# Kernel tuning notes

Measured on AMD Instinct MI355X. Metric: run time of the kernel, lower is better.

Reference implementation:

```python
import jax, jax.numpy as jnp
import numpy as np

BOHR = 1.8897261258369282  # Angstrom -> Bohr, as in SKparam
CUTOFF = 6.0
LATTICE = np.diag([5.0, 5.0, 5.0]).astype(np.float32)
N_ATOMS, N_SPECIES, N_POLY, N_KPT = 512, 4, 12, 32


def _compute_shifts():
    # Exact replica of DFTB.compute_shift in numpy.
    inv = np.linalg.inv(LATTICE)
    n_rep = np.ceil(np.linalg.norm(inv, axis=0) * CUTOFF).astype(int)
    grid = np.stack(np.meshgrid(*[np.arange(-n, n + 1) for n in n_rep], indexing='ij'), -1).reshape(-1, 3)
    a = np.where(grid > 0, grid - 1, grid)
    shrunk = np.where(a < 0, grid + 1, a)              # shrink each component toward 0 by 1
    sh2 = shrunk.astype(np.float32) @ LATTICE           # lattice.T @ r == r @ lattice
    keep = np.linalg.norm(sh2, axis=1) < CUTOFF
    return (grid[keep].astype(np.float32) @ LATTICE)    # [S,3], S=81 for this lattice/cutoff


def setup_inputs() -> dict:
    key = jax.random.key(0)
    k1, k2, k3, k4, k5 = jax.random.split(key, 5)
    positions = jax.random.uniform(k1, (N_ATOMS, 3), dtype=jnp.float32) * 5.0
    species = jax.random.randint(k2, (N_ATOMS,), 0, N_SPECIES)
    kpoints = jax.random.uniform(k3, (N_KPT, 3), dtype=jnp.float32)
    # decaying per-degree scale keeps polyval bounded at x = cutoff*BOHR ~ 11.3
    scale = (1.0 / 12.0) ** jnp.arange(N_POLY, dtype=jnp.float32)
    param_matrix = jax.random.normal(k4, (N_SPECIES, N_SPECIES, N_POLY), dtype=jnp.float32) * scale
    onsite = jax.random.normal(k5, (N_SPECIES,), dtype=jnp.float32)
    shifts = jnp.asarray(_compute_shifts())
    return {"positions": positions, "species": species, "kpoints": kpoints,
            "param_matrix": param_matrix, "onsite": onsite, "shifts": shifts}


def reference(positions, species, kpoints, param_matrix, onsite, shifts):
    # pairwise distance vectors under periodic shifts: [N,N,S,3]
    dvec = positions[None, :, None, :] + shifts[None, None, :, :] - positions[:, :, None][:, None].reshape(-1, 1, 1, 3)
    dvec = positions[None, :, None, :] + shifts[None, None, :, :] - positions[:, None, None, :]
    dr2 = jnp.sum(dvec * dvec, axis=-1)                       # [N,N,S]
    dr = jnp.sqrt(jnp.where(dr2 > 0.0, dr2, 1.0))
    dr = jnp.where(dr2 > 0.0, dr, 0.0)
    x = dr * BOHR
    # species-pair gather of Vsss polynomial coefficients: [N,N,P]
    coeffs = param_matrix[species[:, None], species[None, :]]
    # Horner eval (torch polyval: p[0] is the constant term after fliplr)
    y = jnp.zeros_like(x)
    for k in range(N_POLY - 1, -1, -1):
        y = y * x + coeffs[:, :, k][:, :, None]
    # calc_tb_params mask: zero for onsite (dr<=0.1) and beyond cutoff
    V = jnp.where((dr > 0.1) & (dr <= CUTOFF), y, 0.0)        # [N,N,S]
    # Bloch phases per k-point and shift (calc_phase_matrix, vectorized)
    inv_lat = jnp.asarray(np.linalg.inv(LATTICE))
    kc = kpoints @ inv_lat.T                                   # [K,3]
    ang = (2.0 * np.pi) * (kc @ shifts.T)                      # [K,S]
    Hr = jnp.einsum('ijs,ks->kij', V, jnp.cos(ang))            # [K,N,N]
    Hi = jnp.einsum('ijs,ks->kij', V, jnp.sin(ang))
    Hr = Hr + jnp.diag(onsite[species])[None]                  # onsite diagonal
    return jnp.stack([Hr, Hi])                                 # [2,K,N,N] real view of complex H
```

## Files before the change

kernel.cpp:

```cpp
#include <hip/hip_runtime.h>

#define NATOMS 512
#define N2 (NATOMS*NATOMS)
#define NKPT 32
#define NPOLY 12
#define NSP 4
#define NSMAX 96
#define TJ 256
#define NTHREADS 256
#define SG_STR 260

typedef __attribute__((ext_vector_type(8))) short bf16x8;
typedef __attribute__((ext_vector_type(4))) float f32x4;

static __device__ __forceinline__ unsigned f2bf2(float lo, float hi) {
    union { float f; unsigned u; } a, b; a.f = lo; b.f = hi;
    unsigned ra = a.u + 0x7FFFu + ((a.u >> 16) & 1u);
    unsigned rb = b.u + 0x7FFFu + ((b.u >> 16) & 1u);
    return (ra >> 16) | (rb & 0xFFFF0000u);
}

__global__ void phase_tab(const float* __restrict__ kpoints,
                          const float* __restrict__ shifts,
                          unsigned* __restrict__ Ttg, int ns)
{
    int idx = blockIdx.x * 256 + threadIdx.x;
    if (idx >= 64 * 48) return;
    int row = idx / 48, s2 = idx - row * 48;
    int k = row & 31;
    float kcx = kpoints[k*3]   * 0.2f;
    float kcy = kpoints[k*3+1] * 0.2f;
    float kcz = kpoints[k*3+2] * 0.2f;
    float val[2] = {0.f, 0.f};
    #pragma unroll
    for (int h = 0; h < 2; ++h) {
        int s = 2*s2 + h;
        if (s < ns) {
            float d = (kcx*shifts[s*3] + kcy*shifts[s*3+1]) + kcz*shifts[s*3+2];
            float sn, cs;
            sincosf(6.283185307179586f * d, &sn, &cs);
            val[h] = (row >= 32) ? sn : cs;
        }
    }
    Ttg[idx] = f2bf2(val[0], val[1]);
}

__global__ __launch_bounds__(NTHREADS, 4)
void dftb4(const float* __restrict__ positions,
           const int* __restrict__ species,
           const float* __restrict__ param,
           const float* __restrict__ onsite,
           const float* __restrict__ shifts,
           const unsigned short* __restrict__ Ttg,
           float* __restrict__ out, int ns)
{
    __shared__ float Sg[16][SG_STR];
    __shared__ float4 sh4p[NSMAX + NSMAX/8];
    __shared__ float cpar4[NPOLY*NSP];
    __shared__ float4 pjs[TJ];
    __shared__ int sjs[TJ];

    const int tid = threadIdx.x;
    const int bi = blockIdx.x >> 1;
    const int jt = blockIdx.x & 1;
    if (ns > NSMAX) ns = NSMAX;

    const int si = species[bi];

    {
        int j = jt*TJ + tid;
        pjs[tid] = make_float4(positions[j*3], positions[j*3+1], positions[j*3+2], 0.f);
        sjs[tid] = species[j];
    }
    if (tid < NPOLY*NSP) {
        int q = tid >> 2, sj = tid & 3;
        cpar4[tid] = param[(si*NSP + sj)*NPOLY + q];
    }
    for (int s = tid; s < NSMAX; s += NTHREADS) {
        float4 v = (s < ns)
            ? make_float4(shifts[s*3], shifts[s*3+1], shifts[s*3+2], 0.f)
            : make_float4(1e9f, 1e9f, 1e9f, 0.f);
        sh4p[s + (s >> 3)] = v;
    }
    __syncthreads();

    const int lane = tid & 63, w = tid >> 6;
    const int r16 = lane & 15, g = lane >> 4;

    const float pix = positions[bi*3], piy = positions[bi*3+1], piz = positions[bi*3+2];
    const float ons = onsite[si];

    bf16x8 A[4][3];
    #pragma unroll
    for (int mf = 0; mf < 4; ++mf) {
        const int jl = w*64 + mf*16 + r16;
        const float4 pj = pjs[jl];
        const int sj = sjs[jl];
        float c[NPOLY];
        #pragma unroll
        for (int q = 0; q < NPOLY; ++q) c[q] = cpar4[q*4 + sj];

        #pragma unroll
        for (int kf = 0; kf < 3; ++kf) {
            unsigned pk[4];
            #pragma unroll
            for (int e2 = 0; e2 < 4; ++e2) {
                float v[2];
                #pragma unroll
                for (int h = 0; h < 2; ++h) {
                    const int s = kf*32 + g*8 + e2*2 + h;
                    float4 sh = sh4p[s + (s >> 3)];
                    float dx = (pj.x + sh.x) - pix;
                    float dy = (pj.y + sh.y) - piy;
                    float dz = (pj.z + sh.z) - piz;
                    float dr2 = (__fmul_rn(dx,dx) + __fmul_rn(dy,dy)) + __fmul_rn(dz,dz);
                    float v_ = 0.f;
                    if (dr2 <= 36.001f) {
                        float dr = sqrtf(dr2);
                        if (dr > 0.1f && dr <= 6.0f) {
                            float x = dr * 1.8897261258369282f;
                            float y = c[NPOLY-1];
                            #pragma unroll
                            for (int q = NPOLY-2; q >= 0; --q) y = fmaf(y, x, c[q]);
                            v_ = y;
                        }
                    }
                    v[h] = v_;
                }
                pk[e2] = f2bf2(v[0], v[1]);
            }
            union { unsigned u[4]; bf16x8 v; } au;
            au.u[0] = pk[0]; au.u[1] = pk[1]; au.u[2] = pk[2]; au.u[3] = pk[3];
            A[mf][kf] = au.v;
        }
    }

    const size_t obase = (size_t)bi*NATOMS + (size_t)jt*TJ;
    #pragma unroll
    for (int nf = 0; nf < 4; ++nf) {
        const unsigned short* tb = Ttg + (size_t)(nf*16 + r16)*NSMAX + g*8;
        bf16x8 B0 = *(const bf16x8*)(tb);
        bf16x8 B1 = *(const bf16x8*)(tb + 32);
        bf16x8 B2 = *(const bf16x8*)(tb + 64);

        f32x4 acc[4];
        #pragma unroll
        for (int mf = 0; mf < 4; ++mf) {
            acc[mf] = (f32x4){0.f, 0.f, 0.f, 0.f};
            acc[mf] = __builtin_amdgcn_mfma_f32_16x16x32_bf16(A[mf][0], B0, acc[mf], 0, 0, 0);
            acc[mf] = __builtin_amdgcn_mfma_f32_16x16x32_bf16(A[mf][1], B1, acc[mf], 0, 0, 0);
            acc[mf] = __builtin_amdgcn_mfma_f32_16x16x32_bf16(A[mf][2], B2, acc[mf], 0, 0, 0);
        }

        __syncthreads();
        #pragma unroll
        for (int mf = 0; mf < 4; ++mf)
            *(float4*)&Sg[r16][w*64 + mf*16 + g*4] = *(float4*)&acc[mf];
        __syncthreads();

        #pragma unroll
        for (int q = 0; q < 4; ++q) {
            const int p = w*4 + q;
            const int kcol = nf*16 + p;
            float4 v = *(float4*)&Sg[p][lane*4];
            if (kcol < 32) {
                int d = bi - (int)(jt*TJ + lane*4);
                if (d >= 0 && d < 4) ((float*)&v)[d] += ons;
            }
            *(float4*)(out + (size_t)kcol*N2 + obase + lane*4) = v;
        }
    }
}

extern "C" void kernel_launch(void* const* d_in, const int* in_sizes, int n_in,
                              void* d_out, int out_size, void* d_ws, size_t ws_size,
                              hipStream_t stream) {
    const float* positions = (const float*)d_in[0];
    const int*   species   = (const int*)d_in[1];
    const float* kpoints   = (const float*)d_in[2];
    const float* param     = (const float*)d_in[3];
    const float* onsite    = (const float*)d_in[4];
    const float* shifts    = (const float*)d_in[5];
    int ns = in_sizes[5] / 3;
    float* out = (float*)d_out;
    unsigned* Ttg = (unsigned*)d_ws;

    phase_tab<<<dim3(12), 256, 0, stream>>>(kpoints, shifts, Ttg, ns);
    dim3 grid(NATOMS * (NATOMS/TJ));
    dftb4<<<grid, NTHREADS, 0, stream>>>(positions, species, param, onsite,
                                         shifts, (const unsigned short*)Ttg, out, ns);
}
```

Before: 48.17 us.

## Sort shifts near-first, skip far groups via ballot, shrink tile, store directly

A new single-thread prep kernel reorders the periodic shifts so that near shifts come first and far ones last, padded with sentinels. The main kernel uses a wave-wide ballot to skip the sqrt and polynomial work when no lane in the wave is within the cutoff. It also halves the j-tile to 128 with four blocks per row, raises the launch-bounds occupancy target, and writes MFMA accumulators straight to global memory instead of transposing through shared memory with barriers. Writes are now 16-byte fragments scattered per lane rather than fully coalesced rows, and the extra serial prep kernel adds launch latency.

Measured after the change: 104.8 us. 118% more time.

```diff
diff --git a/kernel.cpp b/kernel.cpp
--- a/kernel.cpp
+++ b/kernel.cpp
@@ -6,9 +6,8 @@
 #define NPOLY 12
 #define NSP 4
 #define NSMAX 96
-#define TJ 256
+#define TJ 128
 #define NTHREADS 256
-#define SG_STR 260
 
 typedef __attribute__((ext_vector_type(8))) short bf16x8;
 typedef __attribute__((ext_vector_type(4))) float f32x4;
@@ -20,8 +19,24 @@
     return (ra >> 16) | (rb & 0xFFFF0000u);
 }
 
+__global__ void prep_shifts(const float* __restrict__ shifts,
+                            float4* __restrict__ shp4, int ns)
+{
+    if (blockIdx.x == 0 && threadIdx.x == 0) {
+        int idx = 0;
+        for (int pass = 0; pass < 2; ++pass)
+            for (int s = 0; s < ns; ++s) {
+                float x = shifts[s*3], y = shifts[s*3+1], z = shifts[s*3+2];
+                float m = fmaxf(fabsf(x), fmaxf(fabsf(y), fabsf(z)));
+                bool far = m > 7.5f;
+                if ((pass == 1) == far) shp4[idx++] = make_float4(x, y, z, 0.f);
+            }
+        for (; idx < NSMAX; ++idx) shp4[idx] = make_float4(1e9f, 1e9f, 1e9f, 0.f);
+    }
+}
+
 __global__ void phase_tab(const float* __restrict__ kpoints,
-                          const float* __restrict__ shifts,
+                          const float4* __restrict__ shp4,
                           unsigned* __restrict__ Ttg, int ns)
 {
     int idx = blockIdx.x * 256 + threadIdx.x;
@@ -36,7 +51,8 @@
     for (int h = 0; h < 2; ++h) {
         int s = 2*s2 + h;
         if (s < ns) {
-            float d = (kcx*shifts[s*3] + kcy*shifts[s*3+1]) + kcz*shifts[s*3+2];
+            float4 sh = shp4[s];
+            float d = (kcx*sh.x + kcy*sh.y) + kcz*sh.z;
             float sn, cs;
             sincosf(6.283185307179586f * d, &sn, &cs);
             val[h] = (row >= 32) ? sn : cs;
@@ -45,29 +61,26 @@
     Ttg[idx] = f2bf2(val[0], val[1]);
 }
 
-__global__ __launch_bounds__(NTHREADS, 4)
-void dftb4(const float* __restrict__ positions,
+__global__ __launch_bounds__(NTHREADS, 6)
+void dftb5(const float* __restrict__ positions,
            const int* __restrict__ species,
            const float* __restrict__ param,
            const float* __restrict__ onsite,
-           const float* __restrict__ shifts,
+           const float4* __restrict__ shp4,
            const unsigned short* __restrict__ Ttg,
-           float* __restrict__ out, int ns)
+           float* __restrict__ out)
 {
-    __shared__ float Sg[16][SG_STR];
     __shared__ float4 sh4p[NSMAX + NSMAX/8];
     __shared__ float cpar4[NPOLY*NSP];
     __shared__ float4 pjs[TJ];
     __shared__ int sjs[TJ];
 
     const int tid = threadIdx.x;
-    const int bi = blockIdx.x >> 1;
-    const int jt = blockIdx.x & 1;
-    if (ns > NSMAX) ns = NSMAX;
-
+    const int bi = blockIdx.x >> 2;
+    const int jt = blockIdx.x & 3;
     const int si = species[bi];
 
-    {
+    if (tid < TJ) {
         int j = jt*TJ + tid;
         pjs[tid] = make_float4(positions[j*3], positions[j*3+1], positions[j*3+2], 0.f);
         sjs[tid] = species[j];
@@ -76,12 +89,8 @@
         int q = tid >> 2, sj = tid & 3;
         cpar4[tid] = param[(si*NSP + sj)*NPOLY + q];
     }
-    for (int s = tid; s < NSMAX; s += NTHREADS) {
-        float4 v = (s < ns)
-            ? make_float4(shifts[s*3], shifts[s*3+1], shifts[s*3+2], 0.f)
-            : make_float4(1e9f, 1e9f, 1e9f, 0.f);
-        sh4p[s + (s >> 3)] = v;
-    }
+    for (int s = tid; s < NSMAX; s += NTHREADS)
+        sh4p[s + (s >> 3)] = shp4[s];
     __syncthreads();
 
     const int lane = tid & 63, w = tid >> 6;
@@ -90,10 +99,10 @@
     const float pix = positions[bi*3], piy = positions[bi*3+1], piz = positions[bi*3+2];
     const float ons = onsite[si];
 
-    bf16x8 A[4][3];
+    bf16x8 A[2][3];
     #pragma unroll
-    for (int mf = 0; mf < 4; ++mf) {
-        const int jl = w*64 + mf*16 + r16;
+    for (int mf = 0; mf < 2; ++mf) {
+        const int jl = w*32 + mf*16 + r16;
         const float4 pj = pjs[jl];
         const int sj = sjs[jl];
         float c[NPOLY];
@@ -114,15 +123,18 @@
                     float dy = (pj.y + sh.y) - piy;
                     float dz = (pj.z + sh.z) - piz;
                     float dr2 = (__fmul_rn(dx,dx) + __fmul_rn(dy,dy)) + __fmul_rn(dz,dz);
+                    bool maybe = (dr2 <= 36.001f);
                     float v_ = 0.f;
-                    if (dr2 <= 36.001f) {
-                        float dr = sqrtf(dr2);
-                        if (dr > 0.1f && dr <= 6.0f) {
-                            float x = dr * 1.8897261258369282f;
-                            float y = c[NPOLY-1];
-                            #pragma unroll
-                            for (int q = NPOLY-2; q >= 0; --q) y = fmaf(y, x, c[q]);
-                            v_ = y;
+                    if (__ballot(maybe) != 0ULL) {
+                        if (maybe) {
+                            float dr = sqrtf(dr2);
+                            if (dr > 0.1f && dr <= 6.0f) {
+                                float x = dr * 1.8897261258369282f;
+                                float y = c[NPOLY-1];
+                                #pragma unroll
+                                for (int q = NPOLY-2; q >= 0; --q) y = fmaf(y, x, c[q]);
+                                v_ = y;
+                            }
                         }
                     }
                     v[h] = v_;
@@ -135,39 +147,27 @@
         }
     }
 
-    const size_t obase = (size_t)bi*NATOMS + (size_t)jt*TJ;
+    const int jbase = jt*TJ + w*32;
     #pragma unroll
     for (int nf = 0; nf < 4; ++nf) {
-        const unsigned short* tb = Ttg + (size_t)(nf*16 + r16)*NSMAX + g*8;
+        const int kcol = nf*16 + r16;
+        const unsigned short* tb = Ttg + (size_t)kcol*NSMAX + g*8;
         bf16x8 B0 = *(const bf16x8*)(tb);
         bf16x8 B1 = *(const bf16x8*)(tb + 32);
         bf16x8 B2 = *(const bf16x8*)(tb + 64);
-
-        f32x4 acc[4];
         #pragma unroll
-        for (int mf = 0; mf < 4; ++mf) {
-            acc[mf] = (f32x4){0.f, 0.f, 0.f, 0.f};
-            acc[mf] = __builtin_amdgcn_mfma_f32_16x16x32_bf16(A[mf][0], B0, acc[mf], 0, 0, 0);
-            acc[mf] = __builtin_amdgcn_mfma_f32_16x16x32_bf16(A[mf][1], B1, acc[mf], 0, 0, 0);
-            acc[mf] = __builtin_amdgcn_mfma_f32_16x16x32_bf16(A[mf][2], B2, acc[mf], 0, 0, 0);
-        }
-
-        __syncthreads();
-        #pragma unroll
-        for (int mf = 0; mf < 4; ++mf)
-            *(float4*)&Sg[r16][w*64 + mf*16 + g*4] = *(float4*)&acc[mf];
-        __syncthreads();
-
-        #pragma unroll
-        for (int q = 0; q < 4; ++q) {
-            const int p = w*4 + q;
-            const int kcol = nf*16 + p;
-            float4 v = *(float4*)&Sg[p][lane*4];
+        for (int mf = 0; mf < 2; ++mf) {
+            f32x4 acc = {0.f, 0.f, 0.f, 0.f};
+            acc = __builtin_amdgcn_mfma_f32_16x16x32_bf16(A[mf][0], B0, acc, 0, 0, 0);
+            acc = __builtin_amdgcn_mfma_f32_16x16x32_bf16(A[mf][1], B1, acc, 0, 0, 0);
+            acc = __builtin_amdgcn_mfma_f32_16x16x32_bf16(A[mf][2], B2, acc, 0, 0, 0);
+            const int jb = jbase + mf*16 + g*4;
+            float4 v; v.x = acc[0]; v.y = acc[1]; v.z = acc[2]; v.w = acc[3];
             if (kcol < 32) {
-                int d = bi - (int)(jt*TJ + lane*4);
+                int d = bi - jb;
                 if (d >= 0 && d < 4) ((float*)&v)[d] += ons;
             }
-            *(float4*)(out + (size_t)kcol*N2 + obase + lane*4) = v;
+            *(float4*)(out + (size_t)kcol*N2 + (size_t)bi*NATOMS + jb) = v;
         }
     }
 }
@@ -183,10 +183,13 @@
     const float* shifts    = (const float*)d_in[5];
     int ns = in_sizes[5] / 3;
     float* out = (float*)d_out;
-    unsigned* Ttg = (unsigned*)d_ws;
 
-    phase_tab<<<dim3(12), 256, 0, stream>>>(kpoints, shifts, Ttg, ns);
+    float4*   shp4 = (float4*)d_ws;
+    unsigned* Ttg  = (unsigned*)((char*)d_ws + 2048);
+
+    prep_shifts<<<dim3(1), 64, 0, stream>>>(shifts, shp4, ns);
+    phase_tab<<<dim3(12), 256, 0, stream>>>(kpoints, shp4, Ttg, ns);
     dim3 grid(NATOMS * (NATOMS/TJ));
-    dftb4<<<grid, NTHREADS, 0, stream>>>(positions, species, param, onsite,
-                                         shifts, (const unsigned short*)Ttg, out, ns);
+    dftb5<<<grid, NTHREADS, 0, stream>>>(positions, species, param, onsite,
+                                         shp4, (const unsigned short*)Ttg, out);
 }
```
